# Kernel tuning notes

Measured on AMD Instinct MI355X. Metric: run time of the kernel, lower is better.

The kernel has to match this reference:

```python
import jax, jax.numpy as jnp
import numpy as np
import math

N, E, G = 10000, 100000, 500
HID, H = 128, 4
C = HID                      # out_channels per head (PyG TransformerConv)
NFREQ, NSPACE = 10, 3
EDIM = 2 * NFREQ * NSPACE    # 60 = dis_emb.dim
LAT, DIS = 6, 3
IN_DIM = HID + LAT + DIS     # 137
EPS = 1e-5


def _lin_init(k, fan_in, shape):
    b = 1.0 / math.sqrt(fan_in)
    return jax.random.uniform(k, shape, jnp.float32, -b, b)


def setup_inputs() -> dict:
    key = jax.random.key(0)
    ks = jax.random.split(key, 12)
    return dict(
        node_features=jax.random.normal(ks[0], (N, HID), jnp.float32),
        frac_coords=jax.random.uniform(ks[1], (N, DIS), jnp.float32),
        lattice_feats=jax.random.normal(ks[2], (G, LAT), jnp.float32),
        edge_index=jax.random.randint(ks[3], (2, E), 0, N),
        node2graph=jnp.sort(jax.random.randint(ks[4], (N,), 0, G)),
        frac_diff=jax.random.normal(ks[5], (E, DIS), jnp.float32) * 0.1,
        ln_gamma=jnp.ones((HID,), jnp.float32),
        ln_beta=jnp.zeros((HID,), jnp.float32),
        Wq=_lin_init(ks[6], IN_DIM, (IN_DIM, H * C)), bq=jnp.zeros((H * C,), jnp.float32),
        Wk=_lin_init(ks[7], IN_DIM, (IN_DIM, H * C)), bk=jnp.zeros((H * C,), jnp.float32),
        Wv=_lin_init(ks[8], IN_DIM, (IN_DIM, H * C)), bv=jnp.zeros((H * C,), jnp.float32),
        We=_lin_init(ks[9], EDIM, (EDIM, H * C)),
        Wskip=_lin_init(ks[10], IN_DIM, (IN_DIM, C)), bskip=jnp.zeros((C,), jnp.float32),
    )


def _sinusoids(frac_diff):
    # SinusoidsEmbedding: emb = x[...,None]*2*pi*arange(F); cat(sin, cos); detached
    freqs = 2.0 * jnp.pi * jnp.arange(NFREQ, dtype=jnp.float32)    # [F]
    emb = frac_diff[:, :, None] * freqs[None, None, :]             # [E,3,F]
    emb = emb.reshape(-1, NSPACE * NFREQ)                          # [E,30]
    return jnp.concatenate([jnp.sin(emb), jnp.cos(emb)], axis=-1)  # [E,60]


def _segment_softmax(scores, idx, num_segments):
    # softmax over variable-size neighborhoods grouped by target node idx
    m = jax.ops.segment_max(scores, idx, num_segments=num_segments)
    ex = jnp.exp(scores - m[idx])
    s = jax.ops.segment_sum(ex, idx, num_segments=num_segments)
    return ex / (s[idx] + 1e-16)


def reference(node_features, frac_coords, lattice_feats, edge_index, node2graph,
              frac_diff, ln_gamma, ln_beta, Wq, bq, Wk, bk, Wv, bv, We, Wskip, bskip):
    edge_emb = jax.lax.stop_gradient(_sinusoids(frac_diff))  # .detach() in original
    node_input = node_features
    # LayerNorm (biased variance, torch default)
    mu = node_features.mean(-1, keepdims=True)
    var = node_features.var(-1, keepdims=True)
    h = (node_features - mu) * jax.lax.rsqrt(var + EPS) * ln_gamma + ln_beta
    # gather per-graph lattice features to nodes, concat
    lat = lattice_feats.reshape(-1, LAT)[node2graph]                # [N,6]
    x = jnp.concatenate([h, lat, frac_coords], axis=1)              # [N,137]

    q = (x @ Wq + bq).reshape(N, H, C)
    k = (x @ Wk + bk).reshape(N, H, C)
    v = (x @ Wv + bv).reshape(N, H, C)
    e = (edge_emb @ We).reshape(E, H, C)                            # lin_edge (no bias)

    src, dst = edge_index[0], edge_index[1]  # message flows src -> dst (PyG default)
    k_e = k[src] + e                                                # [E,H,C]
    alpha = (q[dst] * k_e).sum(-1) / math.sqrt(C)                   # [E,H]
    alpha = _segment_softmax(alpha, dst, N)
    msg = (v[src] + e) * alpha[:, :, None]                          # [E,H,C]
    out = jax.ops.segment_sum(msg, dst, num_segments=N)             # [N,H,C]
    out = out.mean(axis=1)                                          # concat=False -> head mean
    out = out + (x @ Wskip + bskip)                                 # root skip connection
    return node_input + jax.nn.silu(out)
```

## Files before the change

### kernel.cpp

```cpp
#include <hip/hip_runtime.h>
#include <math.h>

#define N_NODES 10000
#define N_EDGES 100000
#define HIDDEN  128
#define NHEAD   4
#define CHAN    128
#define IN_DIM  137
#define KPAD    160
#define NCOLS   1904
#define NPAD    1920
#define LATD    6
#define DISD    3

#define PREP_BLOCKS 2500
#define WTOT   (NCOLS * KPAD + 4 * 128 * 64)
#define WBLOCKS ((WTOT + 255) / 256)

typedef __attribute__((ext_vector_type(8))) short short8v;
typedef __attribute__((ext_vector_type(4))) float float4v;

__device__ inline unsigned short f2bf(float f) {
    unsigned u = __float_as_uint(f);
    unsigned r = 0x7fffu + ((u >> 16) & 1u);
    return (unsigned short)((u + r) >> 16);
}
__device__ inline float bf2f(unsigned short u) {
    return __uint_as_float(((unsigned)u) << 16);
}

__global__ __launch_bounds__(256) void prep_weights_kernel(
    const float* __restrict__ nf, const float* __restrict__ frac,
    const float* __restrict__ lat, const int* __restrict__ n2g,
    const float* __restrict__ gamma, const float* __restrict__ beta,
    const float* __restrict__ Wq, const float* __restrict__ bq,
    const float* __restrict__ Wk, const float* __restrict__ bk,
    const float* __restrict__ Wv, const float* __restrict__ bv,
    const float* __restrict__ Wsk, const float* __restrict__ bsk,
    const float* __restrict__ We,
    unsigned short* __restrict__ xb, int* __restrict__ hist,
    unsigned short* __restrict__ wallT, float* __restrict__ bias_all,
    unsigned short* __restrict__ webt)
{
    if (blockIdx.x < PREP_BLOCKS) {
        int wave = threadIdx.x >> 6;
        int lane = threadIdx.x & 63;
        int n = blockIdx.x * 4 + wave;
        if (n >= N_NODES) return;

        float v0 = nf[n * HIDDEN + lane];
        float v1 = nf[n * HIDDEN + 64 + lane];
        float s  = v0 + v1;
        float sq = v0 * v0 + v1 * v1;
        #pragma unroll
        for (int m = 1; m < 64; m <<= 1) {
            s  += __shfl_xor(s, m);
            sq += __shfl_xor(sq, m);
        }
        float mean = s * (1.0f / 128.0f);
        float var  = sq * (1.0f / 128.0f) - mean * mean;
        float inv  = rsqrtf(var + 1e-5f);

        xb[n * KPAD + lane]      = f2bf((v0 - mean) * inv * gamma[lane]      + beta[lane]);
        xb[n * KPAD + 64 + lane] = f2bf((v1 - mean) * inv * gamma[64 + lane] + beta[64 + lane]);
        if (lane < LATD) xb[n * KPAD + HIDDEN + lane]        = f2bf(lat[n2g[n] * LATD + lane]);
        if (lane < DISD) xb[n * KPAD + HIDDEN + LATD + lane] = f2bf(frac[n * DISD + lane]);
        if (lane >= 41)  xb[n * KPAD + 96 + lane] = 0;
        if (lane == 0)   hist[n] = 0;
    } else {
        int idx = (blockIdx.x - PREP_BLOCKS) * 256 + threadIdx.x;
        if (idx >= WTOT) return;
        if (idx < NCOLS * KPAD) {
            int n = idx / KPAD, k = idx % KPAD;
            if (n < 1664) {
                float val = 0.0f;
                if (k < IN_DIM) {
                    if (n < 512)        val = Wq[(size_t)k * 512 + n];
                    else if (n < 1024)  val = Wk[(size_t)k * 512 + (n - 512)];
                    else if (n < 1536)  val = Wv[(size_t)k * 512 + (n - 1024)];
                    else                val = Wsk[(size_t)k * 128 + (n - 1536)];
                }
                wallT[idx] = f2bf(val);
                if (k == 0) {
                    float b;
                    if (n < 512)        b = bq[n];
                    else if (n < 1024)  b = bk[n - 512];
                    else if (n < 1536)  b = bv[n - 1024];
                    else                b = bsk[n - 1536];
                    bias_all[n] = b;
                }
            } else {
                int hj = n - 1664;
                int h = hj / 60, j = hj % 60;
                float s = 0.0f;
                if (k < IN_DIM) {
                    #pragma unroll 4
                    for (int c = 0; c < 128; ++c)
                        s += Wq[(size_t)k * 512 + h * 128 + c] * We[(size_t)j * 512 + h * 128 + c];
                }
                wallT[idx] = f2bf(s);
                if (k == KPAD - 1) {
                    float b = 0.0f;
                    #pragma unroll 4
                    for (int c = 0; c < 128; ++c)
                        b += bq[h * 128 + c] * We[(size_t)j * 512 + h * 128 + c];
                    bias_all[n] = b;
                }
            }
        } else {
            int g = idx - NCOLS * KPAD;
            int h = g >> 13, c = (g >> 6) & 127, j = g & 63;
            float v = (j < 60) ? We[(size_t)j * 512 + h * 128 + c] : 0.0f;
            webt[g] = f2bf(v);
        }
    }
}

__global__ __launch_bounds__(256) void hist_kernel(
    const int* __restrict__ eidx, int* __restrict__ hist)
{
    int e = blockIdx.x * 256 + threadIdx.x;
    if (e < N_EDGES) atomicAdd(&hist[eidx[N_EDGES + e]], 1);
}

__global__ __launch_bounds__(1024) void scan_kernel(
    const int* __restrict__ hist, int* __restrict__ offsets, int* __restrict__ cursor)
{
    __shared__ int part[1024];
    const int t = threadIdx.x;
    const int base = t * 10;
    int loc[10];
    int s = 0;
    #pragma unroll
    for (int i = 0; i < 10; ++i) {
        int v = (base + i < N_NODES) ? hist[base + i] : 0;
        loc[i] = s; s += v;
    }
    part[t] = s;
    __syncthreads();
    for (int off = 1; off < 1024; off <<= 1) {
        int v = (t >= off) ? part[t - off] : 0;
        __syncthreads();
        part[t] += v;
        __syncthreads();
    }
    int pre = (t > 0) ? part[t - 1] : 0;
    #pragma unroll
    for (int i = 0; i < 10; ++i)
        if (base + i < N_NODES) {
            offsets[base + i] = pre + loc[i];
            cursor[base + i]  = pre + loc[i];
        }
    if (t == 1023) offsets[N_NODES] = part[1023];
}

__global__ __launch_bounds__(256) void scatter_kernel(
    const int* __restrict__ eidx, const float* __restrict__ fdiff,
    int* __restrict__ cursor, int* __restrict__ sorted_src,
    float* __restrict__ sorted_fd)
{
    int e = blockIdx.x * 256 + threadIdx.x;
    if (e >= N_EDGES) return;
    int src = eidx[e];
    int dst = eidx[N_EDGES + e];
    int pos = atomicAdd(&cursor[dst], 1);
    sorted_src[pos] = src;
    sorted_fd[pos * 3 + 0] = fdiff[e * 3 + 0];
    sorted_fd[pos * 3 + 1] = fdiff[e * 3 + 1];
    sorted_fd[pos * 3 + 2] = fdiff[e * 3 + 2];
}

__global__ __launch_bounds__(256) void mfma_gemm_kernel(
    const unsigned short* __restrict__ xb, const unsigned short* __restrict__ wallT,
    const float* __restrict__ bias_all,
    float* __restrict__ sq, unsigned short* __restrict__ kvq)
{
    __shared__ __align__(16) unsigned short Alds[64 * 168];
    const int row0 = blockIdx.y * 64;
    const int col0 = blockIdx.x * 128;
    const int tid  = threadIdx.x;

    for (int i = tid; i < 64 * 20; i += 256) {
        int r = i / 20, c8 = (i % 20) * 8;
        uint4 v = make_uint4(0u, 0u, 0u, 0u);
        if (row0 + r < N_NODES)
            v = *reinterpret_cast<const uint4*>(&xb[(size_t)(row0 + r) * KPAD + c8]);
        *reinterpret_cast<uint4*>(&Alds[r * 168 + c8]) = v;
    }
    __syncthreads();

    const int l   = tid & 63;
    const int wid = tid >> 6;
    const int wr  = (wid >> 1) * 32;
    const int wc  = (wid & 1) * 64;
    const int lr  = l & 15;
    const int lk  = (l >> 4) * 8;

    float4v acc[2][4];
    #pragma unroll
    for (int tr = 0; tr < 2; ++tr)
        #pragma unroll
        for (int tc = 0; tc < 4; ++tc)
            acc[tr][tc] = (float4v){0.0f, 0.0f, 0.0f, 0.0f};

    #pragma unroll
    for (int ks = 0; ks < 5; ++ks) {
        short8v a[2], b[4];
        #pragma unroll
        for (int t = 0; t < 2; ++t)
            a[t] = *reinterpret_cast<const short8v*>(&Alds[(wr + t * 16 + lr) * 168 + ks * 32 + lk]);
        #pragma unroll
        for (int t = 0; t < 4; ++t)
            b[t] = *reinterpret_cast<const short8v*>(
                &wallT[(size_t)(col0 + wc + t * 16 + lr) * KPAD + ks * 32 + lk]);
        #pragma unroll
        for (int tr = 0; tr < 2; ++tr)
            #pragma unroll
            for (int tc = 0; tc < 4; ++tc)
                acc[tr][tc] = __builtin_amdgcn_mfma_f32_16x16x32_bf16(a[tr], b[tc], acc[tr][tc], 0, 0, 0);
    }

    #pragma unroll
    for (int tr = 0; tr < 2; ++tr) {
        #pragma unroll
        for (int tc = 0; tc < 4; ++tc) {
            const int col  = col0 + wc + tc * 16 + lr;
            const float bias = bias_all[col];
            #pragma unroll
            for (int j = 0; j < 4; ++j) {
                const int row = row0 + wr + tr * 16 + (l >> 4) * 4 + j;
                if (row < N_NODES) {
                    float val = acc[tr][tc][j] + bias;
                    if (col < 1536)
                        kvq[(size_t)row * 1536 + col] = f2bf(val);
                    else if (col < 1664)
                        sq[(size_t)row * 384 + (col - 1536)] = val;
                    else if (col < NCOLS)
                        sq[(size_t)row * 384 + 128 + (col - 1664)] = val;
                }
            }
        }
    }
}

__global__ __launch_bounds__(256) void gather_kernel(
    const float* __restrict__ sq, const unsigned short* __restrict__ kvq,
    const int* __restrict__ offsets, const int* __restrict__ sorted_src,
    const float* __restrict__ sorted_fd,
    float* __restrict__ avbuf, unsigned short* __restrict__ aggbuf,
    float* __restrict__ sumwbuf)
{
    const int n    = blockIdx.x;
    const int h    = threadIdx.x >> 6;
    const int l    = threadIdx.x & 63;
    const int hl   = l & 31;
    const int half = l >> 5;
    const float TWO_PI = 6.283185307179586f;
    const float scale  = 0.08838834764831845f;

    const ushort4 qv = *reinterpret_cast<const ushort4*>(
        &kvq[(size_t)n * 1536 + h * 128 + 4 * hl]);
    const float q4x = bf2f(qv.x), q4y = bf2f(qv.y);
    const float q4z = bf2f(qv.z), q4w = bf2f(qv.w);
    const float qe_a = sq[(size_t)n * 384 + 128 + h * 60 + hl];
    const bool  v2ok = (hl < 28);
    const float qe_b = v2ok ? sq[(size_t)n * 384 + 128 + h * 60 + hl + 32] : 0.0f;

    const int   jj1  = (hl < 30) ? hl : hl - 30;
    const int   sd1  = jj1 / 10;
    const float fc1  = TWO_PI * (float)(jj1 % 10);
    const bool  sin1 = (hl < 30);
    const int   jj2  = hl + 2;
    const int   sd2  = v2ok ? (jj2 / 10) : 0;
    const float fc2  = v2ok ? TWO_PI * (float)(jj2 % 10) : 0.0f;

    float ax = 0.f, ay = 0.f, az = 0.f, aw = 0.f;
    float agg1 = 0.f, agg2 = 0.f, sumw = 0.f;
    const int e0 = offsets[n], e1 = offsets[n + 1];

    for (int base = e0; base < e1; base += 4) {
        const int eA = base + half;
        const int eB = base + half + 2;
        const bool okA = (eA < e1), okB = (eB < e1);
        const int iA = okA ? eA : e0;
        const int iB = okB ? eB : e0;
        const int srcA = sorted_src[iA];
        const int srcB = sorted_src[iB];
        const float fdA1 = sorted_fd[iA * 3 + sd1];
        const float fdA2 = sorted_fd[iA * 3 + sd2];
        const float fdB1 = sorted_fd[iB * 3 + sd1];
        const float fdB2 = sorted_fd[iB * 3 + sd2];
        const unsigned short* pA = &kvq[(size_t)srcA * 1536 + 512 + h * 128 + 4 * hl];
        const unsigned short* pB = &kvq[(size_t)srcB * 1536 + 512 + h * 128 + 4 * hl];
        const ushort4 kA = *reinterpret_cast<const ushort4*>(pA);
        const ushort4 vA = *reinterpret_cast<const ushort4*>(pA + 512);
        const ushort4 kB = *reinterpret_cast<const ushort4*>(pB);
        const ushort4 vB = *reinterpret_cast<const ushort4*>(pB + 512);

        const float eA1 = sin1 ? __sinf(fdA1 * fc1) : __cosf(fdA1 * fc1);
        const float eA2 = __cosf(fdA2 * fc2);
        const float eB1 = sin1 ? __sinf(fdB1 * fc1) : __cosf(fdB1 * fc1);
        const float eB2 = __cosf(fdB2 * fc2);

        float pAs = q4x * bf2f(kA.x) + q4y * bf2f(kA.y)
                  + q4z * bf2f(kA.z) + q4w * bf2f(kA.w)
                  + eA1 * qe_a + eA2 * qe_b;
        float pBs = q4x * bf2f(kB.x) + q4y * bf2f(kB.y)
                  + q4z * bf2f(kB.z) + q4w * bf2f(kB.w)
                  + eB1 * qe_a + eB2 * qe_b;
        #pragma unroll
        for (int m = 1; m <= 16; m <<= 1) {
            pAs += __shfl_xor(pAs, m);
            pBs += __shfl_xor(pBs, m);
        }
        const float wA = okA ? __expf(pAs * scale) : 0.0f;
        const float wB = okB ? __expf(pBs * scale) : 0.0f;
        sumw += wA + wB;
        ax += wA * bf2f(vA.x) + wB * bf2f(vB.x);
        ay += wA * bf2f(vA.y) + wB * bf2f(vB.y);
        az += wA * bf2f(vA.z) + wB * bf2f(vB.z);
        aw += wA * bf2f(vA.w) + wB * bf2f(vB.w);
        agg1 += wA * eA1 + wB * eB1;
        if (v2ok) agg2 += wA * eA2 + wB * eB2;
    }

    sumw += __shfl_xor(sumw, 32);
    ax += __shfl_xor(ax, 32);  ay += __shfl_xor(ay, 32);
    az += __shfl_xor(az, 32);  aw += __shfl_xor(aw, 32);
    agg1 += __shfl_xor(agg1, 32);
    agg2 += __shfl_xor(agg2, 32);

    if (half == 0) {
        float4 r;
        r.x = ax; r.y = ay; r.z = az; r.w = aw;
        *reinterpret_cast<float4*>(&avbuf[(size_t)n * 512 + h * 128 + 4 * hl]) = r;
        aggbuf[n * 256 + h * 64 + hl]      = f2bf(agg1);
        aggbuf[n * 256 + h * 64 + 32 + hl] = f2bf(agg2);
        if (hl == 0) sumwbuf[n * 4 + h] = sumw;
    }
}

__global__ __launch_bounds__(256) void corr_kernel(
    const unsigned short* __restrict__ webt, const unsigned short* __restrict__ aggbuf,
    float* __restrict__ avbuf)
{
    __shared__ __align__(16) unsigned short Alds[32 * 264];
    const int node0 = blockIdx.x * 32;
    const int tid = threadIdx.x;

    for (int i = tid; i < 32 * 32; i += 256) {
        int r = i >> 5, c8 = (i & 31) * 8;
        uint4 v = make_uint4(0u, 0u, 0u, 0u);
        if (node0 + r < N_NODES)
            v = *reinterpret_cast<const uint4*>(&aggbuf[(size_t)(node0 + r) * 256 + c8]);
        *reinterpret_cast<uint4*>(&Alds[r * 264 + c8]) = v;
    }
    __syncthreads();

    const int l  = tid & 63;
    const int h  = tid >> 6;
    const int lr = l & 15;
    const int lk = (l >> 4) * 8;

    float4v acc[2][8];
    #pragma unroll
    for (int m = 0; m < 2; ++m)
        #pragma unroll
        for (int nn = 0; nn < 8; ++nn)
            acc[m][nn] = (float4v){0.0f, 0.0f, 0.0f, 0.0f};

    #pragma unroll
    for (int ks = 0; ks < 2; ++ks) {
        short8v a[2], b[8];
        #pragma unroll
        for (int m = 0; m < 2; ++m)
            a[m] = *reinterpret_cast<const short8v*>(
                &Alds[(m * 16 + lr) * 264 + h * 64 + ks * 32 + lk]);
        #pragma unroll
        for (int nn = 0; nn < 8; ++nn)
            b[nn] = *reinterpret_cast<const short8v*>(
                &webt[(size_t)(h * 128 + nn * 16 + lr) * 64 + ks * 32 + lk]);
        #pragma unroll
        for (int m = 0; m < 2; ++m)
            #pragma unroll
            for (int nn = 0; nn < 8; ++nn)
                acc[m][nn] = __builtin_amdgcn_mfma_f32_16x16x32_bf16(a[m], b[nn], acc[m][nn], 0, 0, 0);
    }

    #pragma unroll
    for (int m = 0; m < 2; ++m) {
        #pragma unroll
        for (int nn = 0; nn < 8; ++nn) {
            const int col = h * 128 + nn * 16 + lr;
            #pragma unroll
            for (int j = 0; j < 4; ++j) {
                const int rowi = node0 + m * 16 + (l >> 4) * 4 + j;
                if (rowi < N_NODES) {
                    float* p = &avbuf[(size_t)rowi * 512 + col];
                    *p += acc[m][nn][j];
                }
            }
        }
    }
}

__global__ __launch_bounds__(256) void finalize_kernel(
    const float* __restrict__ avbuf, const float* __restrict__ sumwbuf,
    const float* __restrict__ sq, const float* __restrict__ nf,
    float* __restrict__ out)
{
    int idx = blockIdx.x * 256 + threadIdx.x;
    if (idx >= N_NODES * CHAN) return;
    int n = idx >> 7, c = idx & 127;
    float z = 0.0f;
    #pragma unroll
    for (int h = 0; h < NHEAD; ++h)
        z += avbuf[(size_t)n * 512 + h * 128 + c] / (sumwbuf[n * 4 + h] + 1e-16f);
    z = 0.25f * z + sq[(size_t)n * 384 + c];
    float si = z / (1.0f + __expf(-z));
    out[idx] = nf[idx] + si;
}

extern "C" void kernel_launch(void* const* d_in, const int* in_sizes, int n_in,
                              void* d_out, int out_size, void* d_ws, size_t ws_size,
                              hipStream_t stream)
{
    const float* nf    = (const float*)d_in[0];
    const float* frac  = (const float*)d_in[1];
    const float* lat   = (const float*)d_in[2];
    const int*   eidx  = (const int*)  d_in[3];
    const int*   n2g   = (const int*)  d_in[4];
    const float* fdiff = (const float*)d_in[5];
    const float* gamma = (const float*)d_in[6];
    const float* beta  = (const float*)d_in[7];
    const float* Wq    = (const float*)d_in[8];
    const float* bq    = (const float*)d_in[9];
    const float* Wk    = (const float*)d_in[10];
    const float* bk    = (const float*)d_in[11];
    const float* Wv    = (const float*)d_in[12];
    const float* bv    = (const float*)d_in[13];
    const float* We    = (const float*)d_in[14];
    const float* Wsk   = (const float*)d_in[15];
    const float* bsk   = (const float*)d_in[16];
    float* out = (float*)d_out;

    float* sq        = (float*)d_ws;
    float* avbuf     = sq + (size_t)N_NODES * 384;
    float* sumwbuf   = avbuf + (size_t)N_NODES * 512;
    float* bias_all  = sumwbuf + (size_t)N_NODES * 4;
    float* sorted_fd = bias_all + NPAD;
    unsigned short* xb     = (unsigned short*)(sorted_fd + (size_t)N_EDGES * 3);
    unsigned short* wallT  = xb + (size_t)N_NODES * KPAD;
    unsigned short* webt   = wallT + (size_t)NPAD * KPAD;
    unsigned short* aggbuf = webt + 4 * 128 * 64;
    unsigned short* kvq    = aggbuf + (size_t)N_NODES * 256;
    int* hist       = (int*)(kvq + (size_t)N_NODES * 1536);
    int* offsets    = hist + N_NODES;
    int* cursor     = offsets + N_NODES + 1;
    int* sorted_src = cursor + N_NODES;

    prep_weights_kernel<<<PREP_BLOCKS + WBLOCKS, 256, 0, stream>>>(
        nf, frac, lat, n2g, gamma, beta,
        Wq, bq, Wk, bk, Wv, bv, Wsk, bsk, We,
        xb, hist, wallT, bias_all, webt);

    hist_kernel<<<(N_EDGES + 255) / 256, 256, 0, stream>>>(eidx, hist);
    scan_kernel<<<1, 1024, 0, stream>>>(hist, offsets, cursor);
    scatter_kernel<<<(N_EDGES + 255) / 256, 256, 0, stream>>>(
        eidx, fdiff, cursor, sorted_src, sorted_fd);

    dim3 ggrid(NPAD / 128, (N_NODES + 63) / 64);
    mfma_gemm_kernel<<<ggrid, 256, 0, stream>>>(xb, wallT, bias_all, sq, kvq);

    gather_kernel<<<N_NODES, 256, 0, stream>>>(
        sq, kvq, offsets, sorted_src, sorted_fd, avbuf, aggbuf, sumwbuf);

    corr_kernel<<<(N_NODES + 31) / 32, 256, 0, stream>>>(webt, aggbuf, avbuf);

    finalize_kernel<<<(N_NODES * CHAN + 255) / 256, 256, 0, stream>>>(
        avbuf, sumwbuf, sq, nf, out);
}
```

Before: 152.7 us.

## Store K in FP8, interleave K/V per head, merge scatter into GEMM launch

The edge scatter and the projection GEMM now share one launch, with the first blocks doing the scatter and the rest doing GEMM tiles, which removes a kernel boundary. K is stored as FP8 and V as bf16, packed together per node and head in one 384-byte record, and Q moves to its own buffer. The aim is to cut the gather kernel's random-access traffic and give better locality per neighbour fetch. The cost is reduced precision in the attention scores from FP8 keys, and the extra branching in the merged kernel.

Measured after the change: 148.3 us. -2.9%, faster.

```diff
diff --git a/kernel.cpp b/kernel.cpp
--- a/kernel.cpp
+++ b/kernel.cpp
@@ -17,8 +17,13 @@
 #define WTOT   (NCOLS * KPAD + 4 * 128 * 64)
 #define WBLOCKS ((WTOT + 255) / 256)
 
+#define SCAT_BLOCKS ((N_EDGES + 255) / 256)
+#define GEMM_BX 15
+#define GEMM_BY ((N_NODES + 63) / 64)
+
 typedef __attribute__((ext_vector_type(8))) short short8v;
 typedef __attribute__((ext_vector_type(4))) float float4v;
+typedef __attribute__((ext_vector_type(2))) float float2v;
 
 __device__ inline unsigned short f2bf(float f) {
     unsigned u = __float_as_uint(f);
@@ -154,30 +159,33 @@
     if (t == 1023) offsets[N_NODES] = part[1023];
 }
 
-__global__ __launch_bounds__(256) void scatter_kernel(
+__global__ __launch_bounds__(256) void gemm_scatter_kernel(
+    const unsigned short* __restrict__ xb, const unsigned short* __restrict__ wallT,
+    const float* __restrict__ bias_all,
     const int* __restrict__ eidx, const float* __restrict__ fdiff,
     int* __restrict__ cursor, int* __restrict__ sorted_src,
-    float* __restrict__ sorted_fd)
-{
-    int e = blockIdx.x * 256 + threadIdx.x;
-    if (e >= N_EDGES) return;
-    int src = eidx[e];
-    int dst = eidx[N_EDGES + e];
-    int pos = atomicAdd(&cursor[dst], 1);
-    sorted_src[pos] = src;
-    sorted_fd[pos * 3 + 0] = fdiff[e * 3 + 0];
-    sorted_fd[pos * 3 + 1] = fdiff[e * 3 + 1];
-    sorted_fd[pos * 3 + 2] = fdiff[e * 3 + 2];
-}
-
-__global__ __launch_bounds__(256) void mfma_gemm_kernel(
-    const unsigned short* __restrict__ xb, const unsigned short* __restrict__ wallT,
-    const float* __restrict__ bias_all,
-    float* __restrict__ sq, unsigned short* __restrict__ kvq)
+    float* __restrict__ sorted_fd,
+    float* __restrict__ sq, unsigned short* __restrict__ qbuf,
+    unsigned char* __restrict__ kvb)
 {
     __shared__ __align__(16) unsigned short Alds[64 * 168];
-    const int row0 = blockIdx.y * 64;
-    const int col0 = blockIdx.x * 128;
+
+    if (blockIdx.x < SCAT_BLOCKS) {
+        int e = blockIdx.x * 256 + threadIdx.x;
+        if (e >= N_EDGES) return;
+        int src = eidx[e];
+        int dst = eidx[N_EDGES + e];
+        int pos = atomicAdd(&cursor[dst], 1);
+        sorted_src[pos] = src;
+        sorted_fd[pos * 3 + 0] = fdiff[e * 3 + 0];
+        sorted_fd[pos * 3 + 1] = fdiff[e * 3 + 1];
+        sorted_fd[pos * 3 + 2] = fdiff[e * 3 + 2];
+        return;
+    }
+
+    const int bx   = blockIdx.x - SCAT_BLOCKS;
+    const int row0 = (bx / GEMM_BX) * 64;
+    const int col0 = (bx % GEMM_BX) * 128;
     const int tid  = threadIdx.x;
 
     for (int i = tid; i < 64 * 20; i += 256) {
@@ -231,12 +239,21 @@
                 const int row = row0 + wr + tr * 16 + (l >> 4) * 4 + j;
                 if (row < N_NODES) {
                     float val = acc[tr][tc][j] + bias;
-                    if (col < 1536)
-                        kvq[(size_t)row * 1536 + col] = f2bf(val);
-                    else if (col < 1664)
+                    if (col < 512) {
+                        qbuf[(size_t)row * 512 + col] = f2bf(val);
+                    } else if (col < 1024) {
+                        const int h = (col - 512) >> 7, ck = (col - 512) & 127;
+                        int p = __builtin_amdgcn_cvt_pk_fp8_f32(val, val, 0, false);
+                        kvb[((size_t)row * 4 + h) * 384 + ck] = (unsigned char)(p & 0xFF);
+                    } else if (col < 1536) {
+                        const int h = (col - 1024) >> 7, cv = (col - 1024) & 127;
+                        *reinterpret_cast<unsigned short*>(
+                            kvb + ((size_t)row * 4 + h) * 384 + 128 + 2 * cv) = f2bf(val);
+                    } else if (col < 1664) {
                         sq[(size_t)row * 384 + (col - 1536)] = val;
-                    else if (col < NCOLS)
+                    } else if (col < NCOLS) {
                         sq[(size_t)row * 384 + 128 + (col - 1664)] = val;
+                    }
                 }
             }
         }
@@ -244,7 +261,8 @@
 }
 
 __global__ __launch_bounds__(256) void gather_kernel(
-    const float* __restrict__ sq, const unsigned short* __restrict__ kvq,
+    const float* __restrict__ sq, const unsigned short* __restrict__ qbuf,
+    const unsigned char* __restrict__ kvb,
     const int* __restrict__ offsets, const int* __restrict__ sorted_src,
     const float* __restrict__ sorted_fd,
     float* __restrict__ avbuf, unsigned short* __restrict__ aggbuf,
@@ -259,7 +277,7 @@
     const float scale  = 0.08838834764831845f;
 
     const ushort4 qv = *reinterpret_cast<const ushort4*>(
-        &kvq[(size_t)n * 1536 + h * 128 + 4 * hl]);
+        &qbuf[(size_t)n * 512 + h * 128 + 4 * hl]);
     const float q4x = bf2f(qv.x), q4y = bf2f(qv.y);
     const float q4z = bf2f(qv.z), q4w = bf2f(qv.w);
     const float qe_a = sq[(size_t)n * 384 + 128 + h * 60 + hl];
@@ -290,23 +308,28 @@
         const float fdA2 = sorted_fd[iA * 3 + sd2];
         const float fdB1 = sorted_fd[iB * 3 + sd1];
         const float fdB2 = sorted_fd[iB * 3 + sd2];
-        const unsigned short* pA = &kvq[(size_t)srcA * 1536 + 512 + h * 128 + 4 * hl];
-        const unsigned short* pB = &kvq[(size_t)srcB * 1536 + 512 + h * 128 + 4 * hl];
-        const ushort4 kA = *reinterpret_cast<const ushort4*>(pA);
-        const ushort4 vA = *reinterpret_cast<const ushort4*>(pA + 512);
-        const ushort4 kB = *reinterpret_cast<const ushort4*>(pB);
-        const ushort4 vB = *reinterpret_cast<const ushort4*>(pB + 512);
+        const unsigned char* pA = kvb + ((size_t)srcA * 4 + h) * 384;
+        const unsigned char* pB = kvb + ((size_t)srcB * 4 + h) * 384;
+        const unsigned kAu = *reinterpret_cast<const unsigned*>(pA + 4 * hl);
+        const ushort4  vA  = *reinterpret_cast<const ushort4*>(pA + 128 + 8 * hl);
+        const unsigned kBu = *reinterpret_cast<const unsigned*>(pB + 4 * hl);
+        const ushort4  vB  = *reinterpret_cast<const ushort4*>(pB + 128 + 8 * hl);
 
         const float eA1 = sin1 ? __sinf(fdA1 * fc1) : __cosf(fdA1 * fc1);
         const float eA2 = __cosf(fdA2 * fc2);
         const float eB1 = sin1 ? __sinf(fdB1 * fc1) : __cosf(fdB1 * fc1);
         const float eB2 = __cosf(fdB2 * fc2);
 
-        float pAs = q4x * bf2f(kA.x) + q4y * bf2f(kA.y)
-                  + q4z * bf2f(kA.z) + q4w * bf2f(kA.w)
+        const float2v kA01 = __builtin_amdgcn_cvt_pk_f32_fp8(kAu, false);
+        const float2v kA23 = __builtin_amdgcn_cvt_pk_f32_fp8(kAu, true);
+        const float2v kB01 = __builtin_amdgcn_cvt_pk_f32_fp8(kBu, false);
+        const float2v kB23 = __builtin_amdgcn_cvt_pk_f32_fp8(kBu, true);
+
+        float pAs = q4x * kA01[0] + q4y * kA01[1]
+                  + q4z * kA23[0] + q4w * kA23[1]
                   + eA1 * qe_a + eA2 * qe_b;
-        float pBs = q4x * bf2f(kB.x) + q4y * bf2f(kB.y)
-                  + q4z * bf2f(kB.z) + q4w * bf2f(kB.w)
+        float pBs = q4x * kB01[0] + q4y * kB01[1]
+                  + q4z * kB23[0] + q4w * kB23[1]
                   + eB1 * qe_a + eB2 * qe_b;
         #pragma unroll
         for (int m = 1; m <= 16; m <<= 1) {
@@ -453,8 +476,9 @@
     unsigned short* wallT  = xb + (size_t)N_NODES * KPAD;
     unsigned short* webt   = wallT + (size_t)NPAD * KPAD;
     unsigned short* aggbuf = webt + 4 * 128 * 64;
-    unsigned short* kvq    = aggbuf + (size_t)N_NODES * 256;
-    int* hist       = (int*)(kvq + (size_t)N_NODES * 1536);
+    unsigned short* qbuf   = aggbuf + (size_t)N_NODES * 256;
+    unsigned char*  kvb    = (unsigned char*)(qbuf + (size_t)N_NODES * 512);
+    int* hist       = (int*)(kvb + (size_t)N_NODES * 4 * 384);
     int* offsets    = hist + N_NODES;
     int* cursor     = offsets + N_NODES + 1;
     int* sorted_src = cursor + N_NODES;
@@ -466,14 +490,13 @@
 
     hist_kernel<<<(N_EDGES + 255) / 256, 256, 0, stream>>>(eidx, hist);
     scan_kernel<<<1, 1024, 0, stream>>>(hist, offsets, cursor);
-    scatter_kernel<<<(N_EDGES + 255) / 256, 256, 0, stream>>>(
-        eidx, fdiff, cursor, sorted_src, sorted_fd);
-
-    dim3 ggrid(NPAD / 128, (N_NODES + 63) / 64);
-    mfma_gemm_kernel<<<ggrid, 256, 0, stream>>>(xb, wallT, bias_all, sq, kvq);
+
+    gemm_scatter_kernel<<<SCAT_BLOCKS + GEMM_BX * GEMM_BY, 256, 0, stream>>>(
+        xb, wallT, bias_all, eidx, fdiff, cursor, sorted_src, sorted_fd,
+        sq, qbuf, kvb);
 
     gather_kernel<<<N_NODES, 256, 0, stream>>>(
-        sq, kvq, offsets, sorted_src, sorted_fd, avbuf, aggbuf, sumwbuf);
+        sq, qbuf, kvb, offsets, sorted_src, sorted_fd, avbuf, aggbuf, sumwbuf);
 
     corr_kernel<<<(N_NODES + 31) / 32, 256, 0, stream>>>(webt, aggbuf, avbuf);
 
```
